# Performance work log

Hardware: AMD Instinct MI355X
Metric: run time of the kernel (lower is better)

Reference implementation:

```python
import jax, jax.numpy as jnp
import numpy as np

N_USERS = 100000
N_ITEMS = 150000
N_NODES = N_USERS + N_ITEMS
N_EDGES = 4000000
LATENT_DIM = 64
N_LAYERS = 3


def setup_inputs() -> dict:
    key = jax.random.key(0)
    k1, k2, k3, k4, k5 = jax.random.split(key, 5)
    user_emb = 0.1 * jax.random.normal(k1, (N_USERS, LATENT_DIM), dtype=jnp.float32)
    item_emb = 0.1 * jax.random.normal(k2, (N_ITEMS, LATENT_DIM), dtype=jnp.float32)
    # COO representation of the symmetric-normalized adjacency D^-1/2 A D^-1/2
    edge_src = jax.random.randint(k3, (N_EDGES,), 0, N_NODES, dtype=jnp.int32)
    edge_dst = jax.random.randint(k4, (N_EDGES,), 0, N_NODES, dtype=jnp.int32)
    edge_vals = jax.random.uniform(k5, (N_EDGES,), dtype=jnp.float32)
    return {"user_emb": user_emb, "item_emb": item_emb, "edge_vals": edge_vals,
            "edge_src": edge_src, "edge_dst": edge_dst}


def _spmm(edge_src, edge_dst, edge_vals, x):
    # y[dst] += val * x[src]  (equivalent of torch.sparse.mm(graph, x))
    msgs = edge_vals[:, None] * x[edge_src]  # [E, d]
    return jax.ops.segment_sum(msgs, edge_dst, num_segments=N_NODES)


def reference(user_emb, item_emb, edge_vals, edge_src, edge_dst):
    # LightGCN.computer(): n_layers of SpMM propagation + layer-stack mean pool
    all_emb = jnp.concatenate([user_emb, item_emb], axis=0)  # [N, d]
    acc = all_emb  # running sum over layer stack (layer 0)
    x = all_emb
    for _ in range(N_LAYERS):
        x = _spmm(edge_src, edge_dst, edge_vals, x)
        acc = acc + x
    light_out = acc / jnp.asarray(N_LAYERS + 1, dtype=acc.dtype)
    users = light_out[:N_USERS]
    items = light_out[N_USERS:]
    return users, items
```

## Files before the change

### kernel.cpp

```cpp
#include <hip/hip_runtime.h>
#include <hip/hip_bf16.h>

#define N_USERS 100000
#define N_ITEMS 150000
#define N_NODES 250000
#define N_EDGES 4000000
#define DIM     64
#define N_ELEM  (N_NODES * DIM)
#define U_ELEM  (N_USERS * DIM)
#define BSHIFT  8
#define NBUCKET ((N_NODES + (1 << BSHIFT) - 1) >> BSHIFT)
#define NB_HIST 2048
#define CHUNK   ((N_EDGES + NB_HIST - 1) / NB_HIST)
#define KPL     (NB_HIST / 64)

__device__ __forceinline__ float bflo(unsigned int u) { return __uint_as_float(u << 16); }
__device__ __forceinline__ float bfhi(unsigned int u) { return __uint_as_float(u & 0xffff0000u); }
__device__ __forceinline__ unsigned int bfr(float f) {
    unsigned int u = __float_as_uint(f);
    return (u + 0x7fffu + ((u >> 16) & 1u)) >> 16;
}
__device__ __forceinline__ unsigned int pk(float a, float b) {
    return bfr(a) | (bfr(b) << 16);
}

__global__ void probe_dtype(const unsigned short* __restrict__ ue, int* __restrict__ flag) {
    int lane = threadIdx.x;
    int bad = 0;
    #pragma unroll
    for (int k = 0; k < 8; ++k) {
        unsigned int b = ((unsigned int)ue[lane * 8 + k]) << 16;
        float f = fabsf(__uint_as_float(b));
        if (!(f < 1.0f)) bad = 1;
    }
    unsigned long long m = __ballot(bad);
    if (lane == 0) flag[0] = (m == 0ULL) ? 1 : 0;
}

__global__ void hist_bucket(const int* __restrict__ dst, int* __restrict__ M) {
    __shared__ int h[NBUCKET];
    for (int b = threadIdx.x; b < NBUCKET; b += blockDim.x) h[b] = 0;
    __syncthreads();
    int base = blockIdx.x * CHUNK;
    for (int i = threadIdx.x; i < CHUNK; i += blockDim.x) {
        int e = base + i;
        if (e < N_EDGES) atomicAdd(&h[dst[e] >> BSHIFT], 1);
    }
    __syncthreads();
    for (int b = threadIdx.x; b < NBUCKET; b += blockDim.x)
        M[blockIdx.x * NBUCKET + b] = h[b];
}

__global__ void col_sum(const int* __restrict__ M, int* __restrict__ tot) {
    int lane = threadIdx.x & 63;
    int b = (blockIdx.x * blockDim.x + threadIdx.x) >> 6;
    if (b >= NBUCKET) return;
    int s = 0;
    #pragma unroll 8
    for (int k = lane; k < NB_HIST; k += 64) s += M[k * NBUCKET + b];
    #pragma unroll
    for (int off = 32; off; off >>= 1) s += __shfl_xor(s, off);
    if (lane == 0) tot[b] = s;
}

__global__ void scan_bbase(const int* __restrict__ tot, int* __restrict__ bbase,
                           int* __restrict__ row_ptr) {
    __shared__ int sh[1024];
    int b = threadIdx.x;
    int v = (b < NBUCKET) ? tot[b] : 0;
    sh[b] = v;
    __syncthreads();
    for (int off = 1; off < 1024; off <<= 1) {
        int t = (b >= off) ? sh[b - off] : 0;
        __syncthreads();
        sh[b] += t;
        __syncthreads();
    }
    if (b < NBUCKET) bbase[b] = sh[b] - v;
    if (b == 0) { bbase[NBUCKET] = N_EDGES; row_ptr[N_NODES] = N_EDGES; }
}

__global__ void row_base(int* __restrict__ M, const int* __restrict__ bbase) {
    int lane = threadIdx.x & 63;
    int b = (blockIdx.x * blockDim.x + threadIdx.x) >> 6;
    if (b >= NBUCKET) return;
    int k0 = lane * KPL;
    int v[KPL];
    int s = 0;
    #pragma unroll
    for (int j = 0; j < KPL; ++j) { v[j] = M[(k0 + j) * NBUCKET + b]; s += v[j]; }
    int p = s;
    #pragma unroll
    for (int off = 1; off < 64; off <<= 1) {
        int t = __shfl_up(p, off);
        if (lane >= off) p += t;
    }
    int run = bbase[b] + p - s;
    #pragma unroll
    for (int j = 0; j < KPL; ++j) { M[(k0 + j) * NBUCKET + b] = run; run += v[j]; }
}

__global__ void bin_scatter(const int* __restrict__ src, const int* __restrict__ dst,
                            const void* __restrict__ valsv, const int* __restrict__ flag,
                            const int* __restrict__ M, int2* __restrict__ aux) {
    __shared__ int cur[NBUCKET];
    for (int b = threadIdx.x; b < NBUCKET; b += blockDim.x)
        cur[b] = M[blockIdx.x * NBUCKET + b];
    __syncthreads();
    const int isbf = *flag;
    int base = blockIdx.x * CHUNK;
    for (int i = threadIdx.x; i < CHUNK; i += blockDim.x) {
        int e = base + i;
        if (e >= N_EDGES) break;
        int d = dst[e];
        int pos = atomicAdd(&cur[d >> BSHIFT], 1);
        float v = isbf ? __bfloat162float(((const __hip_bfloat16*)valsv)[e])
                       : ((const float*)valsv)[e];
        int2 r;
        r.x = src[e] | ((d & ((1 << BSHIFT) - 1)) << 18);
        r.y = __float_as_int(v);
        aux[pos] = r;
    }
}

__global__ void bucket_csr(const int* __restrict__ bbase, const int2* __restrict__ aux,
                           int* __restrict__ row_ptr, int2* __restrict__ sedge) {
    __shared__ int h[256];
    __shared__ int c[256];
    int b  = blockIdx.x;
    int n0 = b << BSHIFT;
    int nd = N_NODES - n0; if (nd > 256) nd = 256;
    int lo = bbase[b], hi = bbase[b + 1];
    int t = threadIdx.x;
    h[t] = 0;
    __syncthreads();
    for (int e = lo + t; e < hi; e += blockDim.x)
        atomicAdd(&h[(aux[e].x >> 18) & 255], 1);
    __syncthreads();
    int v = h[t];
    c[t] = v;
    __syncthreads();
    for (int off = 1; off < 256; off <<= 1) {
        int u = (t >= off) ? c[t - off] : 0;
        __syncthreads();
        c[t] += u;
        __syncthreads();
    }
    int gbase = lo + c[t] - v;
    if (t < nd) row_ptr[n0 + t] = gbase;
    c[t] = gbase;
    __syncthreads();
    for (int e = lo + t; e < hi; e += blockDim.x) {
        int2 r = aux[e];
        int pos = atomicAdd(&c[(r.x >> 18) & 255], 1);
        int2 o; o.x = r.x & 0x3FFFF; o.y = r.y;
        sedge[pos] = o;
    }
}

__global__ void init_kernel(const void* __restrict__ uev, const void* __restrict__ iev,
                            const int* __restrict__ flag,
                            __hip_bfloat16* __restrict__ x,
                            void* __restrict__ outacc) {
    int i4 = blockIdx.x * blockDim.x + threadIdx.x;
    if (i4 >= N_ELEM / 4) return;
    const int isbf = *flag;
    float v0, v1, v2, v3;
    if (i4 < U_ELEM / 4) {
        if (isbf) {
            uint2 u = ((const uint2*)uev)[i4];
            v0 = bflo(u.x); v1 = bfhi(u.x); v2 = bflo(u.y); v3 = bfhi(u.y);
        } else {
            float4 f = ((const float4*)uev)[i4];
            v0 = f.x; v1 = f.y; v2 = f.z; v3 = f.w;
        }
    } else {
        int j4 = i4 - U_ELEM / 4;
        if (isbf) {
            uint2 u = ((const uint2*)iev)[j4];
            v0 = bflo(u.x); v1 = bfhi(u.x); v2 = bflo(u.y); v3 = bfhi(u.y);
        } else {
            float4 f = ((const float4*)iev)[j4];
            v0 = f.x; v1 = f.y; v2 = f.z; v3 = f.w;
        }
    }
    uint2 pv; pv.x = pk(v0, v1); pv.y = pk(v2, v3);
    ((uint2*)x)[i4] = pv;
    if (outacc) {
        if (isbf) {
            uint2 o; o.x = pk(0.25f * v0, 0.25f * v1); o.y = pk(0.25f * v2, 0.25f * v3);
            ((uint2*)outacc)[i4] = o;
        } else {
            float4 f; f.x = 0.25f * v0; f.y = 0.25f * v1; f.z = 0.25f * v2; f.w = 0.25f * v3;
            ((float4*)outacc)[i4] = f;
        }
    }
}

template <int MODE>
__global__ void spmm_csr(const int* __restrict__ row_ptr,
                         const int2* __restrict__ sedge,
                         const __hip_bfloat16* __restrict__ x,
                         __hip_bfloat16* __restrict__ xn,
                         const __hip_bfloat16* __restrict__ p0,
                         const __hip_bfloat16* __restrict__ p1,
                         void* __restrict__ outv,
                         const int* __restrict__ flag) {
    int lane = threadIdx.x & 63;
    int g = lane >> 3;
    int q = lane & 7;
    int w = (blockIdx.x * blockDim.x + threadIdx.x) >> 6;
    if (w >= N_NODES) return;
    int beg = row_ptr[w], end = row_ptr[w + 1];

    const uint4* xo = (const uint4*)x;
    float s0 = 0.f, s1 = 0.f, s2 = 0.f, s3 = 0.f, s4 = 0.f, s5 = 0.f, s6 = 0.f, s7 = 0.f;
    float t0 = 0.f, t1 = 0.f, t2 = 0.f, t3 = 0.f, t4 = 0.f, t5 = 0.f, t6 = 0.f, t7 = 0.f;

    int e0 = beg;
    for (; e0 + 16 <= end; e0 += 16) {
        int2 ra = sedge[e0 + g];
        int2 rb = sedge[e0 + 8 + g];
        uint4 va = xo[(size_t)ra.x * 8 + q];
        uint4 vb = xo[(size_t)rb.x * 8 + q];
        float wa = __int_as_float(ra.y), wb = __int_as_float(rb.y);
        s0 += wa * bflo(va.x); s1 += wa * bfhi(va.x);
        s2 += wa * bflo(va.y); s3 += wa * bfhi(va.y);
        s4 += wa * bflo(va.z); s5 += wa * bfhi(va.z);
        s6 += wa * bflo(va.w); s7 += wa * bfhi(va.w);
        t0 += wb * bflo(vb.x); t1 += wb * bfhi(vb.x);
        t2 += wb * bflo(vb.y); t3 += wb * bfhi(vb.y);
        t4 += wb * bflo(vb.z); t5 += wb * bfhi(vb.z);
        t6 += wb * bflo(vb.w); t7 += wb * bfhi(vb.w);
    }
    for (; e0 < end; e0 += 8) {
        int ee = e0 + g;
        int2 r = sedge[(ee < end) ? ee : (end - 1)];
        float wv = (ee < end) ? __int_as_float(r.y) : 0.f;
        uint4 v = xo[(size_t)r.x * 8 + q];
        s0 += wv * bflo(v.x); s1 += wv * bfhi(v.x);
        s2 += wv * bflo(v.y); s3 += wv * bfhi(v.y);
        s4 += wv * bflo(v.z); s5 += wv * bfhi(v.z);
        s6 += wv * bflo(v.w); s7 += wv * bfhi(v.w);
    }
    s0 += t0; s1 += t1; s2 += t2; s3 += t3;
    s4 += t4; s5 += t5; s6 += t6; s7 += t7;

    s0 += __shfl_xor(s0, 8);  s1 += __shfl_xor(s1, 8);
    s2 += __shfl_xor(s2, 8);  s3 += __shfl_xor(s3, 8);
    s4 += __shfl_xor(s4, 8);  s5 += __shfl_xor(s5, 8);
    s6 += __shfl_xor(s6, 8);  s7 += __shfl_xor(s7, 8);
    s0 += __shfl_xor(s0, 16); s1 += __shfl_xor(s1, 16);
    s2 += __shfl_xor(s2, 16); s3 += __shfl_xor(s3, 16);
    s4 += __shfl_xor(s4, 16); s5 += __shfl_xor(s5, 16);
    s6 += __shfl_xor(s6, 16); s7 += __shfl_xor(s7, 16);
    s0 += __shfl_xor(s0, 32); s1 += __shfl_xor(s1, 32);
    s2 += __shfl_xor(s2, 32); s3 += __shfl_xor(s3, 32);
    s4 += __shfl_xor(s4, 32); s5 += __shfl_xor(s5, 32);
    s6 += __shfl_xor(s6, 32); s7 += __shfl_xor(s7, 32);

    if (g != 0) return;
    size_t oq = (size_t)w * 8 + q;

    if (MODE == 0) {
        uint4 pv;
        pv.x = pk(s0, s1); pv.y = pk(s2, s3); pv.z = pk(s4, s5); pv.w = pk(s6, s7);
        ((uint4*)xn)[oq] = pv;
    } else if (MODE == 1) {
        uint4 a = ((const uint4*)p0)[oq];
        uint4 b = ((const uint4*)p1)[oq];
        uint4 c = ((const uint4*)x)[oq];
        float r0 = 0.25f * (s0 + bflo(a.x) + bflo(b.x) + bflo(c.x));
        float r1 = 0.25f * (s1 + bfhi(a.x) + bfhi(b.x) + bfhi(c.x));
        float r2 = 0.25f * (s2 + bflo(a.y) + bflo(b.y) + bflo(c.y));
        float r3 = 0.25f * (s3 + bfhi(a.y) + bfhi(b.y) + bfhi(c.y));
        float r4 = 0.25f * (s4 + bflo(a.z) + bflo(b.z) + bflo(c.z));
        float r5 = 0.25f * (s5 + bfhi(a.z) + bfhi(b.z) + bfhi(c.z));
        float r6 = 0.25f * (s6 + bflo(a.w) + bflo(b.w) + bflo(c.w));
        float r7 = 0.25f * (s7 + bfhi(a.w) + bfhi(b.w) + bfhi(c.w));
        if (*flag) {
            uint4 pv;
            pv.x = pk(r0, r1); pv.y = pk(r2, r3); pv.z = pk(r4, r5); pv.w = pk(r6, r7);
            ((uint4*)outv)[oq] = pv;
        } else {
            float4 f0; f0.x = r0; f0.y = r1; f0.z = r2; f0.w = r3;
            float4 f1; f1.x = r4; f1.y = r5; f1.z = r6; f1.w = r7;
            ((float4*)outv)[2 * oq]     = f0;
            ((float4*)outv)[2 * oq + 1] = f1;
        }
    } else if (MODE == 2) {
        uint4 pv;
        pv.x = pk(s0, s1); pv.y = pk(s2, s3); pv.z = pk(s4, s5); pv.w = pk(s6, s7);
        ((uint4*)xn)[oq] = pv;
        if (*flag) {
            uint4 ov = ((uint4*)outv)[oq];
            float r0 = bflo(ov.x) + 0.25f * s0;
            float r1 = bfhi(ov.x) + 0.25f * s1;
            float r2 = bflo(ov.y) + 0.25f * s2;
            float r3 = bfhi(ov.y) + 0.25f * s3;
            float r4 = bflo(ov.z) + 0.25f * s4;
            float r5 = bfhi(ov.z) + 0.25f * s5;
            float r6 = bflo(ov.w) + 0.25f * s6;
            float r7 = bfhi(ov.w) + 0.25f * s7;
            uint4 nv;
            nv.x = pk(r0, r1); nv.y = pk(r2, r3); nv.z = pk(r4, r5); nv.w = pk(r6, r7);
            ((uint4*)outv)[oq] = nv;
        } else {
            float4 o0 = ((float4*)outv)[2 * oq];
            float4 o1 = ((float4*)outv)[2 * oq + 1];
            o0.x += 0.25f * s0; o0.y += 0.25f * s1; o0.z += 0.25f * s2; o0.w += 0.25f * s3;
            o1.x += 0.25f * s4; o1.y += 0.25f * s5; o1.z += 0.25f * s6; o1.w += 0.25f * s7;
            ((float4*)outv)[2 * oq]     = o0;
            ((float4*)outv)[2 * oq + 1] = o1;
        }
    } else {
        if (*flag) {
            uint4 ov = ((uint4*)outv)[oq];
            float r0 = bflo(ov.x) + 0.25f * s0;
            float r1 = bfhi(ov.x) + 0.25f * s1;
            float r2 = bflo(ov.y) + 0.25f * s2;
            float r3 = bfhi(ov.y) + 0.25f * s3;
            float r4 = bflo(ov.z) + 0.25f * s4;
            float r5 = bfhi(ov.z) + 0.25f * s5;
            float r6 = bflo(ov.w) + 0.25f * s6;
            float r7 = bfhi(ov.w) + 0.25f * s7;
            uint4 nv;
            nv.x = pk(r0, r1); nv.y = pk(r2, r3); nv.z = pk(r4, r5); nv.w = pk(r6, r7);
            ((uint4*)outv)[oq] = nv;
        } else {
            float4 o0 = ((float4*)outv)[2 * oq];
            float4 o1 = ((float4*)outv)[2 * oq + 1];
            o0.x += 0.25f * s0; o0.y += 0.25f * s1; o0.z += 0.25f * s2; o0.w += 0.25f * s3;
            o1.x += 0.25f * s4; o1.y += 0.25f * s5; o1.z += 0.25f * s6; o1.w += 0.25f * s7;
            ((float4*)outv)[2 * oq]     = o0;
            ((float4*)outv)[2 * oq + 1] = o1;
        }
    }
}

static inline size_t align256(size_t x) { return (x + 255) & ~(size_t)255; }

extern "C" void kernel_launch(void* const* d_in, const int* in_sizes, int n_in,
                              void* d_out, int out_size, void* d_ws, size_t ws_size,
                              hipStream_t stream) {
    const int* es = (const int*)d_in[3];
    const int* ed = (const int*)d_in[4];

    char* wsb = (char*)d_ws;
    size_t off = 0;
    int*  flag    = (int*)wsb;               off = align256(off + sizeof(int));
    int*  M       = (int*)(wsb + off);       off = align256(off + (size_t)NB_HIST * NBUCKET * 4);
    int*  bbase   = (int*)(wsb + off);       off = align256(off + (size_t)(NBUCKET + 1) * 4);
    int*  tot     = (int*)(wsb + off);       off = align256(off + (size_t)NBUCKET * 4);
    int*  row_ptr = (int*)(wsb + off);       off = align256(off + (size_t)(N_NODES + 1) * 4);
    int2* sedge   = (int2*)(wsb + off);      off = align256(off + (size_t)N_EDGES * 8);
    size_t z_off = off;
    int2* aux = (int2*)(wsb + z_off);

    const size_t bfbuf = (size_t)N_ELEM * sizeof(__hip_bfloat16);

    const int eb = 256;
    const int egrid = (N_ELEM / 4 + eb - 1) / eb;
    const int sgrid = (N_NODES + 3) / 4;
    const int wgrid = (NBUCKET + 3) / 4;

    probe_dtype<<<1, 64, 0, stream>>>((const unsigned short*)d_in[0], flag);
    hist_bucket<<<NB_HIST, eb, 0, stream>>>(ed, M);
    col_sum<<<wgrid, eb, 0, stream>>>(M, tot);
    scan_bbase<<<1, 1024, 0, stream>>>(tot, bbase, row_ptr);
    row_base<<<wgrid, eb, 0, stream>>>(M, bbase);
    bin_scatter<<<NB_HIST, eb, 0, stream>>>(es, ed, d_in[2], flag, M, aux);
    bucket_csr<<<NBUCKET, eb, 0, stream>>>(bbase, aux, row_ptr, sedge);

    size_t need_t1 = z_off + 3 * bfbuf;

    if (ws_size >= need_t1) {
        __hip_bfloat16* x0 = (__hip_bfloat16*)(wsb + z_off);
        __hip_bfloat16* x1 = x0 + N_ELEM;
        __hip_bfloat16* x2 = x1 + N_ELEM;
        init_kernel<<<egrid, eb, 0, stream>>>(d_in[0], d_in[1], flag, x0, nullptr);
        spmm_csr<0><<<sgrid, eb, 0, stream>>>(row_ptr, sedge, x0, x1, nullptr, nullptr, nullptr, flag);
        spmm_csr<0><<<sgrid, eb, 0, stream>>>(row_ptr, sedge, x1, x2, nullptr, nullptr, nullptr, flag);
        spmm_csr<1><<<sgrid, eb, 0, stream>>>(row_ptr, sedge, x2, nullptr, x0, x1, d_out, flag);
    } else {
        __hip_bfloat16* x  = (__hip_bfloat16*)(wsb + z_off);
        __hip_bfloat16* xn = x + N_ELEM;
        init_kernel<<<egrid, eb, 0, stream>>>(d_in[0], d_in[1], flag, x, d_out);
        spmm_csr<2><<<sgrid, eb, 0, stream>>>(row_ptr, sedge, x,  xn, nullptr, nullptr, d_out, flag);
        spmm_csr<2><<<sgrid, eb, 0, stream>>>(row_ptr, sedge, xn, x,  nullptr, nullptr, d_out, flag);
        spmm_csr<3><<<sgrid, eb, 0, stream>>>(row_ptr, sedge, x,  nullptr, nullptr, nullptr, d_out, flag);
    }
}
```

Baseline: 637.8 us.

## Replace column-sum and row-base kernels with global atomics for bucket offsets

```diff
diff --git a/kernel.cpp b/kernel.cpp
--- a/kernel.cpp
+++ b/kernel.cpp
@@ -12,7 +12,6 @@
 #define NBUCKET ((N_NODES + (1 << BSHIFT) - 1) >> BSHIFT)
 #define NB_HIST 2048
 #define CHUNK   ((N_EDGES + NB_HIST - 1) / NB_HIST)
-#define KPL     (NB_HIST / 64)
 
 __device__ __forceinline__ float bflo(unsigned int u) { return __uint_as_float(u << 16); }
 __device__ __forceinline__ float bfhi(unsigned int u) { return __uint_as_float(u & 0xffff0000u); }
@@ -24,8 +23,10 @@
     return bfr(a) | (bfr(b) << 16);
 }
 
-__global__ void probe_dtype(const unsigned short* __restrict__ ue, int* __restrict__ flag) {
+__global__ void probe_dtype(const unsigned short* __restrict__ ue, int* __restrict__ flag,
+                            int* __restrict__ tot) {
     int lane = threadIdx.x;
+    for (int b = lane; b < NBUCKET; b += 64) tot[b] = 0;
     int bad = 0;
     #pragma unroll
     for (int k = 0; k < 8; ++k) {
@@ -37,7 +38,8 @@
     if (lane == 0) flag[0] = (m == 0ULL) ? 1 : 0;
 }
 
-__global__ void hist_bucket(const int* __restrict__ dst, int* __restrict__ M) {
+__global__ void hist_bucket(const int* __restrict__ dst, int* __restrict__ M,
+                            int* __restrict__ tot) {
     __shared__ int h[NBUCKET];
     for (int b = threadIdx.x; b < NBUCKET; b += blockDim.x) h[b] = 0;
     __syncthreads();
@@ -47,24 +49,15 @@
         if (e < N_EDGES) atomicAdd(&h[dst[e] >> BSHIFT], 1);
     }
     __syncthreads();
-    for (int b = threadIdx.x; b < NBUCKET; b += blockDim.x)
-        M[blockIdx.x * NBUCKET + b] = h[b];
-}
-
-__global__ void col_sum(const int* __restrict__ M, int* __restrict__ tot) {
-    int lane = threadIdx.x & 63;
-    int b = (blockIdx.x * blockDim.x + threadIdx.x) >> 6;
-    if (b >= NBUCKET) return;
-    int s = 0;
-    #pragma unroll 8
-    for (int k = lane; k < NB_HIST; k += 64) s += M[k * NBUCKET + b];
-    #pragma unroll
-    for (int off = 32; off; off >>= 1) s += __shfl_xor(s, off);
-    if (lane == 0) tot[b] = s;
+    for (int b = threadIdx.x; b < NBUCKET; b += blockDim.x) {
+        int c = h[b];
+        M[blockIdx.x * NBUCKET + b] = c;
+        if (c) atomicAdd(&tot[b], c);
+    }
 }
 
 __global__ void scan_bbase(const int* __restrict__ tot, int* __restrict__ bbase,
-                           int* __restrict__ row_ptr) {
+                           int* __restrict__ gres, int* __restrict__ row_ptr) {
     __shared__ int sh[1024];
     int b = threadIdx.x;
     int v = (b < NBUCKET) ? tot[b] : 0;
@@ -76,36 +69,23 @@
         sh[b] += t;
         __syncthreads();
     }
-    if (b < NBUCKET) bbase[b] = sh[b] - v;
+    if (b < NBUCKET) {
+        int ex = sh[b] - v;
+        bbase[b] = ex;
+        gres[b]  = ex;
+    }
     if (b == 0) { bbase[NBUCKET] = N_EDGES; row_ptr[N_NODES] = N_EDGES; }
-}
-
-__global__ void row_base(int* __restrict__ M, const int* __restrict__ bbase) {
-    int lane = threadIdx.x & 63;
-    int b = (blockIdx.x * blockDim.x + threadIdx.x) >> 6;
-    if (b >= NBUCKET) return;
-    int k0 = lane * KPL;
-    int v[KPL];
-    int s = 0;
-    #pragma unroll
-    for (int j = 0; j < KPL; ++j) { v[j] = M[(k0 + j) * NBUCKET + b]; s += v[j]; }
-    int p = s;
-    #pragma unroll
-    for (int off = 1; off < 64; off <<= 1) {
-        int t = __shfl_up(p, off);
-        if (lane >= off) p += t;
-    }
-    int run = bbase[b] + p - s;
-    #pragma unroll
-    for (int j = 0; j < KPL; ++j) { M[(k0 + j) * NBUCKET + b] = run; run += v[j]; }
 }
 
 __global__ void bin_scatter(const int* __restrict__ src, const int* __restrict__ dst,
                             const void* __restrict__ valsv, const int* __restrict__ flag,
-                            const int* __restrict__ M, int2* __restrict__ aux) {
+                            const int* __restrict__ M, int* __restrict__ gres,
+                            int2* __restrict__ aux) {
     __shared__ int cur[NBUCKET];
-    for (int b = threadIdx.x; b < NBUCKET; b += blockDim.x)
-        cur[b] = M[blockIdx.x * NBUCKET + b];
+    for (int b = threadIdx.x; b < NBUCKET; b += blockDim.x) {
+        int c = M[blockIdx.x * NBUCKET + b];
+        cur[b] = c ? atomicAdd(&gres[b], c) : 0;
+    }
     __syncthreads();
     const int isbf = *flag;
     int base = blockIdx.x * CHUNK;
@@ -352,6 +332,7 @@
     int*  M       = (int*)(wsb + off);       off = align256(off + (size_t)NB_HIST * NBUCKET * 4);
     int*  bbase   = (int*)(wsb + off);       off = align256(off + (size_t)(NBUCKET + 1) * 4);
     int*  tot     = (int*)(wsb + off);       off = align256(off + (size_t)NBUCKET * 4);
+    int*  gres    = (int*)(wsb + off);       off = align256(off + (size_t)NBUCKET * 4);
     int*  row_ptr = (int*)(wsb + off);       off = align256(off + (size_t)(N_NODES + 1) * 4);
     int2* sedge   = (int2*)(wsb + off);      off = align256(off + (size_t)N_EDGES * 8);
     size_t z_off = off;
@@ -362,14 +343,11 @@
     const int eb = 256;
     const int egrid = (N_ELEM / 4 + eb - 1) / eb;
     const int sgrid = (N_NODES + 3) / 4;
-    const int wgrid = (NBUCKET + 3) / 4;
-
-    probe_dtype<<<1, 64, 0, stream>>>((const unsigned short*)d_in[0], flag);
-    hist_bucket<<<NB_HIST, eb, 0, stream>>>(ed, M);
-    col_sum<<<wgrid, eb, 0, stream>>>(M, tot);
-    scan_bbase<<<1, 1024, 0, stream>>>(tot, bbase, row_ptr);
-    row_base<<<wgrid, eb, 0, stream>>>(M, bbase);
-    bin_scatter<<<NB_HIST, eb, 0, stream>>>(es, ed, d_in[2], flag, M, aux);
+
+    probe_dtype<<<1, 64, 0, stream>>>((const unsigned short*)d_in[0], flag, tot);
+    hist_bucket<<<NB_HIST, eb, 0, stream>>>(ed, M, tot);
+    scan_bbase<<<1, 1024, 0, stream>>>(tot, bbase, gres, row_ptr);
+    bin_scatter<<<NB_HIST, eb, 0, stream>>>(es, ed, d_in[2], flag, M, gres, aux);
     bucket_csr<<<NBUCKET, eb, 0, stream>>>(bbase, aux, row_ptr, sedge);
 
     size_t need_t1 = z_off + 3 * bfbuf;
```

Result: slower. 691.1 us (+8.4%).
